# Kernel optimization log

Hardware: AMD Instinct MI355X
Metric: run time of the kernel (lower is better)

## Reference

```python
import jax, jax.numpy as jnp
import numpy as np

NUM_ENTITY = 100000
NUM_TYPE = 5000
DIM = 128
BATCH = 512
MARGIN = 2.0


def setup_inputs() -> dict:
    key = jax.random.key(0)
    k1, k2, k3 = jax.random.split(key, 3)
    x_batch = jax.random.randint(k1, (BATCH,), 0, NUM_ENTITY)
    # xavier_uniform-style init for embedding tables
    lim_e = float(np.sqrt(6.0 / (NUM_ENTITY + DIM)))
    lim_t = float(np.sqrt(6.0 / (NUM_TYPE + DIM)))
    ent_table = jax.random.uniform(k2, (NUM_ENTITY, DIM), minval=-lim_e, maxval=lim_e, dtype=jnp.float32)
    type_table = jax.random.uniform(k3, (NUM_TYPE, DIM), minval=-lim_t, maxval=lim_t, dtype=jnp.float32)
    # padding_idx=0 rows are zero in torch Embedding
    ent_table = ent_table.at[0].set(0.0)
    type_table = type_table.at[0].set(0.0)
    return {"ent_table": ent_table, "type_table": type_table, "x_batch": x_batch}


def reference(ent_table, type_table, x_batch):
    # [B, D] entity embedding lookup
    e = ent_table[x_batch]
    # L1 distance from each entity to every type embedding: [B, T]
    dist = jnp.sum(jnp.abs(e[:, None, :] - type_table[None, :, :]), axis=2)
    return jax.nn.sigmoid(MARGIN - dist)
```

## Files before the change

kernel.cpp:

```cpp
#include <hip/hip_runtime.h>
#include <math.h>

#define NUM_ENTITY 100000
#define NUM_TYPE   5000
#define DIM        128
#define BATCH      512
#define MARGIN     2.0f

#define TG 64
#define BB 32
#define BG 8
#define TSTRIDE 68

typedef _Float16 half_t;
typedef half_t half2_t __attribute__((ext_vector_type(2)));

__device__ __forceinline__ uint32_t pk2(float x, float y) {
    return __builtin_bit_cast(uint32_t, __builtin_amdgcn_cvt_pkrtz(x, y));
}

__device__ __forceinline__ float absdot(uint32_t eu, uint32_t tu, float acc) {
    const half2_t ones = {(half_t)1.0f, (half_t)1.0f};
    half2_t d = __builtin_bit_cast(half2_t, eu) - __builtin_bit_cast(half2_t, tu);
    const uint32_t du = __builtin_bit_cast(uint32_t, d) & 0x7fff7fffu;
#if __has_builtin(__builtin_amdgcn_fdot2)
    return __builtin_amdgcn_fdot2(__builtin_bit_cast(half2_t, du), ones, acc, false);
#else
    half2_t a = __builtin_bit_cast(half2_t, du);
    return acc + (float)a[0] + (float)a[1];
#endif
}

__global__ __launch_bounds__(256, 1) void l1dist_sigmoid_kernel(
    const float* __restrict__ ent,
    const float* __restrict__ typ,
    const int*   __restrict__ xb,
    float*       __restrict__ out)
{
    __shared__ uint32_t tL[TG * TSTRIDE];
    __shared__ uint32_t eL[BB * 64];

    const int tid = threadIdx.x;
    const int l   = tid & 63;
    const int w   = tid >> 6;
    const int t0  = blockIdx.x * TG;
    const int b0  = blockIdx.y * BB;

#pragma unroll
    for (int s = 0; s < 4; ++s) {
        const int g   = tid + 256 * s;
        const int row = g >> 5;
        const int c4  = g & 31;
        const int er  = xb[b0 + row];
        const float4 v = *(const float4*)&ent[er * DIM + c4 * 4];
        uint2 pw;
        pw.x = pk2(v.x, v.y);
        pw.y = pk2(v.z, v.w);
        *(uint2*)&eL[row * 64 + c4 * 2] = pw;
    }

#pragma unroll
    for (int s = 0; s < 8; ++s) {
        const int g   = tid + 256 * s;
        const int row = g >> 5;
        const int c4  = g & 31;
        const int tr  = min(t0 + row, NUM_TYPE - 1);
        const float4 v = *(const float4*)&typ[tr * DIM + c4 * 4];
        uint2 pw;
        pw.x = pk2(v.x, v.y);
        pw.y = pk2(v.z, v.w);
        *(uint2*)&tL[row * TSTRIDE + c4 * 2] = pw;
    }

    __syncthreads();

    uint4 tf[16];
#pragma unroll
    for (int c = 0; c < 16; ++c)
        tf[c] = *(const uint4*)&tL[l * TSTRIDE + c * 4];

    const bool valid = (t0 + l) < NUM_TYPE;
    const int  wb    = w * BG;

#pragma unroll 1
    for (int i = 0; i < BG; ++i) {
        float acc = 0.0f;
#pragma unroll
        for (int c = 0; c < 16; ++c) {
            const uint4 ev = *(const uint4*)&eL[(wb + i) * 64 + c * 4];
            acc = absdot(ev.x, tf[c].x, acc);
            acc = absdot(ev.y, tf[c].y, acc);
            acc = absdot(ev.z, tf[c].z, acc);
            acc = absdot(ev.w, tf[c].w, acc);
        }
        if (valid) {
            const float x = MARGIN - acc;
            out[(b0 + wb + i) * NUM_TYPE + t0 + l] = 1.0f / (1.0f + __expf(-x));
        }
    }
}

extern "C" void kernel_launch(void* const* d_in, const int* in_sizes, int n_in,
                              void* d_out, int out_size, void* d_ws, size_t ws_size,
                              hipStream_t stream) {
    const float* ent = (const float*)d_in[0];
    const float* typ = (const float*)d_in[1];
    const int*   xb  = (const int*)d_in[2];
    float*       out = (float*)d_out;

    dim3 grid((NUM_TYPE + TG - 1) / TG, BATCH / BB);
    dim3 block(256);
    l1dist_sigmoid_kernel<<<grid, block, 0, stream>>>(ent, typ, xb, out);
}
```

Baseline: 26.07 us.

## Pre-gather entity rows to f16 workspace and read them from global memory

Adds a separate kernel that gathers the batch's entity rows once, converts them to packed f16, and writes them to a workspace buffer. The main kernel then skips its per-block entity gather and LDS staging and reads the entity values through wave-uniform global loads. This removes the gather repeated by all 79 type-tile blocks per batch tile. In exchange it adds a second kernel launch, and every inner-loop iteration now does a global/cache load instead of an LDS load. A fallback to the old fused kernel runs when the workspace is too small.

```diff
diff --git a/kernel.cpp b/kernel.cpp
--- a/kernel.cpp
+++ b/kernel.cpp
@@ -31,7 +31,73 @@
 #endif
 }
 
+__global__ __launch_bounds__(64, 1) void egather_f16_kernel(
+    const float* __restrict__ ent,
+    const int*   __restrict__ xb,
+    uint32_t*    __restrict__ ws)
+{
+    const int row = blockIdx.x;
+    const int l   = threadIdx.x;
+    const int er  = xb[row];
+    const float2 v = *(const float2*)&ent[er * DIM + 2 * l];
+    ws[row * 64 + l] = pk2(v.x, v.y);
+}
+
 __global__ __launch_bounds__(256, 1) void l1dist_sigmoid_kernel(
+    const float*    __restrict__ typ,
+    const uint32_t* __restrict__ ew,
+    float*          __restrict__ out)
+{
+    __shared__ uint32_t tL[TG * TSTRIDE];
+
+    const int tid = threadIdx.x;
+    const int l   = tid & 63;
+    const int t0  = blockIdx.x * TG;
+    const int b0  = blockIdx.y * BB;
+
+#pragma unroll
+    for (int s = 0; s < 8; ++s) {
+        const int g   = tid + 256 * s;
+        const int row = g >> 5;
+        const int c4  = g & 31;
+        const int tr  = min(t0 + row, NUM_TYPE - 1);
+        const float4 v = *(const float4*)&typ[tr * DIM + c4 * 4];
+        uint2 pw;
+        pw.x = pk2(v.x, v.y);
+        pw.y = pk2(v.z, v.w);
+        *(uint2*)&tL[row * TSTRIDE + c4 * 2] = pw;
+    }
+    __syncthreads();
+
+    uint4 tf[16];
+#pragma unroll
+    for (int c = 0; c < 16; ++c)
+        tf[c] = *(const uint4*)&tL[l * TSTRIDE + c * 4];
+
+    const bool valid = (t0 + l) < NUM_TYPE;
+    const int wb = __builtin_amdgcn_readfirstlane((tid >> 6) * BG);
+
+#pragma unroll 1
+    for (int i = 0; i < BG; ++i) {
+        const int brow = b0 + wb + i;
+        const uint32_t* er = &ew[brow * 64];
+        float acc = 0.0f;
+#pragma unroll
+        for (int c = 0; c < 16; ++c) {
+            const uint4 ev = *(const uint4*)&er[c * 4];
+            acc = absdot(ev.x, tf[c].x, acc);
+            acc = absdot(ev.y, tf[c].y, acc);
+            acc = absdot(ev.z, tf[c].z, acc);
+            acc = absdot(ev.w, tf[c].w, acc);
+        }
+        if (valid) {
+            const float x = MARGIN - acc;
+            out[brow * NUM_TYPE + t0 + l] = 1.0f / (1.0f + __expf(-x));
+        }
+    }
+}
+
+__global__ __launch_bounds__(256, 1) void l1dist_fallback_kernel(
     const float* __restrict__ ent,
     const float* __restrict__ typ,
     const int*   __restrict__ xb,
@@ -48,30 +114,22 @@
 
 #pragma unroll
     for (int s = 0; s < 4; ++s) {
-        const int g   = tid + 256 * s;
-        const int row = g >> 5;
-        const int c4  = g & 31;
-        const int er  = xb[b0 + row];
+        const int g = tid + 256 * s;
+        const int row = g >> 5, c4 = g & 31;
+        const int er = xb[b0 + row];
         const float4 v = *(const float4*)&ent[er * DIM + c4 * 4];
-        uint2 pw;
-        pw.x = pk2(v.x, v.y);
-        pw.y = pk2(v.z, v.w);
+        uint2 pw; pw.x = pk2(v.x, v.y); pw.y = pk2(v.z, v.w);
         *(uint2*)&eL[row * 64 + c4 * 2] = pw;
     }
-
 #pragma unroll
     for (int s = 0; s < 8; ++s) {
-        const int g   = tid + 256 * s;
-        const int row = g >> 5;
-        const int c4  = g & 31;
-        const int tr  = min(t0 + row, NUM_TYPE - 1);
+        const int g = tid + 256 * s;
+        const int row = g >> 5, c4 = g & 31;
+        const int tr = min(t0 + row, NUM_TYPE - 1);
         const float4 v = *(const float4*)&typ[tr * DIM + c4 * 4];
-        uint2 pw;
-        pw.x = pk2(v.x, v.y);
-        pw.y = pk2(v.z, v.w);
+        uint2 pw; pw.x = pk2(v.x, v.y); pw.y = pk2(v.z, v.w);
         *(uint2*)&tL[row * TSTRIDE + c4 * 2] = pw;
     }
-
     __syncthreads();
 
     uint4 tf[16];
@@ -81,7 +139,6 @@
 
     const bool valid = (t0 + l) < NUM_TYPE;
     const int  wb    = w * BG;
-
 #pragma unroll 1
     for (int i = 0; i < BG; ++i) {
         float acc = 0.0f;
@@ -108,7 +165,14 @@
     const int*   xb  = (const int*)d_in[2];
     float*       out = (float*)d_out;
 
-    dim3 grid((NUM_TYPE + TG - 1) / TG, BATCH / BB);
-    dim3 block(256);
-    l1dist_sigmoid_kernel<<<grid, block, 0, stream>>>(ent, typ, xb, out);
+    const size_t ws_needed = (size_t)BATCH * 64 * sizeof(uint32_t);
+    if (ws_size >= ws_needed) {
+        uint32_t* ew = (uint32_t*)d_ws;
+        egather_f16_kernel<<<dim3(BATCH), dim3(64), 0, stream>>>(ent, xb, ew);
+        dim3 grid((NUM_TYPE + TG - 1) / TG, BATCH / BB);
+        l1dist_sigmoid_kernel<<<grid, dim3(256), 0, stream>>>(typ, ew, out);
+    } else {
+        dim3 grid((NUM_TYPE + TG - 1) / TG, BATCH / BB);
+        l1dist_fallback_kernel<<<grid, dim3(256), 0, stream>>>(ent, typ, xb, out);
+    }
 }
```

After: 30.44 us. 16.8% more time.
